# Optimization experiments

Measured on AMD Instinct MI355X. Metric: run time of the kernel, lower is better.

The kernel has to match this reference:

```python
import math
import jax, jax.numpy as jnp
import numpy as np

B, S, D_MODEL, H = 2, 2048, 1024, 16
D_HEAD = D_MODEL // H
NEG = -90000000000.0


def setup_inputs() -> dict:
    key = jax.random.key(0)
    ks = jax.random.split(key, 12)
    scale = 1.0 / math.sqrt(D_MODEL)
    return {
        "Q": jax.random.normal(ks[0], (B, S, D_MODEL), jnp.float32),
        "K": jax.random.normal(ks[1], (B, S, D_MODEL), jnp.float32),
        "V": jax.random.normal(ks[2], (B, S, D_MODEL), jnp.float32),
        "mask": jax.random.randint(ks[3], (B, 1, S, S), 0, 2).astype(bool),
        "Wq": jax.random.normal(ks[4], (D_MODEL, D_MODEL), jnp.float32) * scale,
        "bq": jnp.zeros((D_MODEL,), jnp.float32),
        "Wk": jax.random.normal(ks[5], (D_MODEL, D_MODEL), jnp.float32) * scale,
        "bk": jnp.zeros((D_MODEL,), jnp.float32),
        "Wv": jax.random.normal(ks[6], (D_MODEL, D_MODEL), jnp.float32) * scale,
        "bv": jnp.zeros((D_MODEL,), jnp.float32),
        "Wo": jax.random.normal(ks[7], (D_MODEL, D_MODEL), jnp.float32) * scale,
        "bo": jnp.zeros((D_MODEL,), jnp.float32),
    }


def _split_heads(x):
    # (B, S, D) -> (B, H, S, Dh)
    b, s, _ = x.shape
    return x.reshape(b, s, H, D_HEAD).transpose(0, 2, 1, 3)


def reference(Q, K, V, mask, Wq, bq, Wk, bk, Wv, bv, Wo, bo):
    q = _split_heads(Q @ Wq.T + bq)
    k = _split_heads(K @ Wk.T + bk)
    v = _split_heads(V @ Wv.T + bv)
    # scaled dot product with additive mask (mask.float() * -9e10)
    scores = jnp.einsum("bhqd,bhkd->bhqk", q, k) / math.sqrt(D_HEAD)
    scores = scores + mask.astype(scores.dtype) * NEG
    attn = jax.nn.softmax(scores, axis=-1)
    ctx = jnp.einsum("bhqk,bhkd->bhqd", attn, v)  # (B, H, S, Dh)
    ctx = ctx.transpose(0, 2, 1, 3).reshape(Q.shape[0], q.shape[2], D_MODEL)
    return ctx @ Wo.T + bo
```

## Files before the change

### kernel.cpp

```cpp
#include <hip/hip_runtime.h>
#include <hip/hip_bf16.h>


typedef __bf16 bf16x8 __attribute__((ext_vector_type(8)));
typedef __bf16 bf16x4 __attribute__((ext_vector_type(4)));
typedef float f32x4 __attribute__((ext_vector_type(4)));

#define S_LEN 2048
#define DM 1024
#define NH 16
#define DH 64
#define MROWS 4096

#define QSCALE 0.18033688011112042f

static __device__ __forceinline__ unsigned short f2bf(float f) {
    __bf16 b = (__bf16)f;
    unsigned short u; __builtin_memcpy(&u, &b, 2); return u;
}

static __device__ __forceinline__ float exp2_hw(float x) {
#if __has_builtin(__builtin_amdgcn_exp2f)
    return __builtin_amdgcn_exp2f(x);
#else
    float r; asm("v_exp_f32 %0, %1" : "=v"(r) : "v"(x)); return r;
#endif
}

static __device__ __forceinline__ unsigned cvtpk_bf16(float lo, float hi) {
    unsigned r;
    asm("v_cvt_pk_bf16_f32 %0, %1, %2" : "=v"(r) : "v"(lo), "v"(hi));
    return r;
}
static __device__ __forceinline__ void pl32swap(unsigned &x, unsigned &y) {
    asm volatile("v_permlane32_swap_b32 %0, %1" : "+v"(x), "+v"(y));
}
static __device__ __forceinline__ void pl16swap(unsigned &x, unsigned &y) {
    asm volatile("v_permlane16_swap_b32 %0, %1" : "+v"(x), "+v"(y));
}

static __device__ __forceinline__ bf16x8 cvt8(float4 a, float4 b) {
    bf16x8 o;
    o[0] = (__bf16)a.x; o[1] = (__bf16)a.y; o[2] = (__bf16)a.z; o[3] = (__bf16)a.w;
    o[4] = (__bf16)b.x; o[5] = (__bf16)b.y; o[6] = (__bf16)b.z; o[7] = (__bf16)b.w;
    return o;
}

__global__ __launch_bounds__(256)
void prep(const int* __restrict__ m, unsigned* __restrict__ mb,
          const float* __restrict__ Q, unsigned short* __restrict__ dQ,
          const float* __restrict__ K, unsigned short* __restrict__ dK,
          const float* __restrict__ V, unsigned short* __restrict__ dV,
          const float* __restrict__ W0, unsigned short* __restrict__ dW0,
          const float* __restrict__ W1, unsigned short* __restrict__ dW1,
          const float* __restrict__ W2, unsigned short* __restrict__ dW2,
          const float* __restrict__ W3, unsigned short* __restrict__ dW3)
{
    const int bx = blockIdx.x, tid = threadIdx.x;
    if (bx < 1024) {
        const int lane = tid & 63, w = tid >> 6;
        const int row = bx * 4 + w;
        const int* src = m + (size_t)row * S_LEN;
        unsigned* dst = mb + (size_t)row * (S_LEN / 32);
        for (int i = 0; i < 32; i++) {
            int v = src[i * 64 + lane];
            unsigned long long bm = __ballot(v != 0);
            if (lane == 0) { dst[i*2] = (unsigned)bm; dst[i*2+1] = (unsigned)(bm >> 32); }
        }
    } else if (bx < 7168) {
        int t = bx - 1024;
        int which = t >> 11;
        const float* s = which == 0 ? Q : which == 1 ? K : V;
        unsigned short* d = which == 0 ? dQ : which == 1 ? dK : dV;
        int i = ((t & 2047) * 256 + tid) * 8;
        float4 a = *(const float4*)(s + i);
        float4 b = *(const float4*)(s + i + 4);
        *(bf16x8*)(d + i) = cvt8(a, b);
    } else {
        int t = bx - 7168;
        int which = t >> 9;
        const float* s = which == 0 ? W0 : which == 1 ? W1 : which == 2 ? W2 : W3;
        unsigned short* d = which == 0 ? dW0 : which == 1 ? dW1 : which == 2 ? dW2 : dW3;
        int i = ((t & 511) * 256 + tid) * 8;
        float4 a = *(const float4*)(s + i);
        float4 b = *(const float4*)(s + i + 4);
        *(bf16x8*)(d + i) = cvt8(a, b);
    }
}

__global__ __launch_bounds__(256)
void gemm128(const unsigned short* __restrict__ X0, const unsigned short* __restrict__ X1,
             const unsigned short* __restrict__ X2,
             const unsigned short* __restrict__ W0, const unsigned short* __restrict__ W1,
             const unsigned short* __restrict__ W2,
             const float* __restrict__ b0, const float* __restrict__ b1,
             const float* __restrict__ b2,
             unsigned short* __restrict__ d0, unsigned short* __restrict__ d1,
             unsigned short* __restrict__ d2)
{
    __shared__ __align__(16) unsigned short As[2][128 * 32];
    __shared__ __align__(16) unsigned short Bs[2][128 * 32];

    const int bid = blockIdx.x + blockIdx.y * 8 + blockIdx.z * 256;
    const int xcd = bid & 7;
    const int t   = bid >> 3;
    const int z   = t >> 5;
    const int u   = t & 31;
    const int nt  = u & 7;
    const int mt  = xcd * 4 + (u >> 3);

    const unsigned short* X = z == 0 ? X0 : z == 1 ? X1 : X2;
    const unsigned short* W = z == 0 ? W0 : z == 1 ? W1 : W2;
    const float* bias        = z == 0 ? b0 : z == 1 ? b1 : b2;
    unsigned short* dstb     = z == 0 ? d0 : z == 1 ? d1 : d2;

    const int tid  = threadIdx.x;
    const int m0   = mt * 128;
    const int n0   = nt * 128;
    const int lane = tid & 63;
    const int w    = tid >> 6;
    const int wm   = (w >> 1) * 64, wn = (w & 1) * 64;
    const int lr   = lane & 15;
    const int lg   = lane >> 4;

    const int srow = tid >> 2, sc8 = (tid & 3) * 8;
    const int srow1 = (tid + 256) >> 2, sc81 = ((tid + 256) & 3) * 8;

    f32x4 acc[4][4];
#pragma unroll
    for (int i = 0; i < 4; i++)
#pragma unroll
        for (int j = 0; j < 4; j++) acc[i][j] = f32x4{0.f, 0.f, 0.f, 0.f};

#define G128_STAGE(buf, kk)                                                          \
    do {                                                                             \
        __builtin_amdgcn_global_load_lds(                                            \
            (const __attribute__((address_space(1))) unsigned*)&X[(size_t)(m0 + srow) * DM + (kk) + sc8],   \
            (__attribute__((address_space(3))) unsigned*)&As[buf][tid * 8], 16, 0, 0);                      \
        __builtin_amdgcn_global_load_lds(                                            \
            (const __attribute__((address_space(1))) unsigned*)&W[(size_t)(n0 + srow) * DM + (kk) + sc8],   \
            (__attribute__((address_space(3))) unsigned*)&Bs[buf][tid * 8], 16, 0, 0);                      \
        __builtin_amdgcn_global_load_lds(                                            \
            (const __attribute__((address_space(1))) unsigned*)&X[(size_t)(m0 + srow1) * DM + (kk) + sc81], \
            (__attribute__((address_space(3))) unsigned*)&As[buf][(tid + 256) * 8], 16, 0, 0);              \
        __builtin_amdgcn_global_load_lds(                                            \
            (const __attribute__((address_space(1))) unsigned*)&W[(size_t)(n0 + srow1) * DM + (kk) + sc81], \
            (__attribute__((address_space(3))) unsigned*)&Bs[buf][(tid + 256) * 8], 16, 0, 0);              \
    } while (0)

    G128_STAGE(0, 0);
    __syncthreads();

    for (int k0 = 0; k0 < DM; k0 += 32) {
        const int cur = (k0 >> 5) & 1;
        if (k0 + 32 < DM) G128_STAGE(cur ^ 1, k0 + 32);

        bf16x8 af[4], bfr[4];
#pragma unroll
        for (int mi = 0; mi < 4; mi++)
            af[mi] = *(const bf16x8*)(&As[cur][(wm + mi * 16 + lr) * 32 + lg * 8]);
#pragma unroll
        for (int ni = 0; ni < 4; ni++)
            bfr[ni] = *(const bf16x8*)(&Bs[cur][(wn + ni * 16 + lr) * 32 + lg * 8]);
#pragma unroll
        for (int mi = 0; mi < 4; mi++)
#pragma unroll
            for (int ni = 0; ni < 4; ni++)
                acc[mi][ni] = __builtin_amdgcn_mfma_f32_16x16x32_bf16(
                    af[mi], bfr[ni], acc[mi][ni], 0, 0, 0);
        __syncthreads();
    }
#undef G128_STAGE

#pragma unroll
    for (int mi = 0; mi < 4; mi++) {
#pragma unroll
        for (int ni = 0; ni < 4; ni++) {
            const int gcol = n0 + wn + ni * 16 + lr;
            const float bv = bias[gcol];
            const int grow0 = m0 + wm + mi * 16 + lg * 4;
            if (z == 2) {
                int b = grow0 >> 11, s = grow0 & (S_LEN - 1);
                int h = gcol >> 6, dh = gcol & 63;
                bf16x4 pk;
#pragma unroll
                for (int r = 0; r < 4; r++) pk[r] = (__bf16)(acc[mi][ni][r] + bv);
                size_t di = ((size_t)(b * NH + h) * DH + dh) * S_LEN + s;
                *(bf16x4*)(&dstb[di]) = pk;
            } else {
#pragma unroll
                for (int r = 0; r < 4; r++) {
                    int grow = grow0 + r;
                    float v = acc[mi][ni][r] + bv;
                    if (z == 0) v *= QSCALE;
                    int b = grow >> 11, s = grow & (S_LEN - 1);
                    int h = gcol >> 6, dh = gcol & 63;
                    dstb[((size_t)(b * NH + h) * S_LEN + s) * DH + dh] = f2bf(v);
                }
            }
        }
    }
}

__global__ __launch_bounds__(256, 2)
void gemm_out(const unsigned short* __restrict__ X, const unsigned short* __restrict__ W,
              const float* __restrict__ bias, float* __restrict__ dst)
{
    __shared__ __align__(16) unsigned short As[2][128 * 32];
    __shared__ __align__(16) unsigned short Bs[2][64 * 32];

    const int bid = blockIdx.x + blockIdx.y * 16;
    const int xcd = bid & 7;
    const int u   = bid >> 3;
    const int nt  = u & 15;
    const int mt  = xcd * 4 + (u >> 4);

    const int tid  = threadIdx.x;
    const int m0   = mt * 128;
    const int n0   = nt * 64;
    const int lane = tid & 63;
    const int w    = tid >> 6;
    const int wm   = (w >> 1) * 64, wn = (w & 1) * 32;
    const int lr   = lane & 15;
    const int lg   = lane >> 4;

    const int srow = tid >> 2, sc8 = (tid & 3) * 8;
    const int srow1 = (tid + 256) >> 2, sc81 = ((tid + 256) & 3) * 8;

    f32x4 acc[4][2];
#pragma unroll
    for (int i = 0; i < 4; i++)
#pragma unroll
        for (int j = 0; j < 2; j++) acc[i][j] = f32x4{0.f, 0.f, 0.f, 0.f};

#define GOUT_STAGE(buf, kk)                                                          \
    do {                                                                             \
        __builtin_amdgcn_global_load_lds(                                            \
            (const __attribute__((address_space(1))) unsigned*)&X[(size_t)(m0 + srow) * DM + (kk) + sc8],   \
            (__attribute__((address_space(3))) unsigned*)&As[buf][tid * 8], 16, 0, 0);                      \
        __builtin_amdgcn_global_load_lds(                                            \
            (const __attribute__((address_space(1))) unsigned*)&X[(size_t)(m0 + srow1) * DM + (kk) + sc81], \
            (__attribute__((address_space(3))) unsigned*)&As[buf][(tid + 256) * 8], 16, 0, 0);              \
        __builtin_amdgcn_global_load_lds(                                            \
            (const __attribute__((address_space(1))) unsigned*)&W[(size_t)(n0 + srow) * DM + (kk) + sc8],   \
            (__attribute__((address_space(3))) unsigned*)&Bs[buf][tid * 8], 16, 0, 0);                      \
    } while (0)

    GOUT_STAGE(0, 0);
    __syncthreads();

    for (int k0 = 0; k0 < DM; k0 += 32) {
        const int cur = (k0 >> 5) & 1;
        if (k0 + 32 < DM) GOUT_STAGE(cur ^ 1, k0 + 32);

        bf16x8 af[4], bfr[2];
#pragma unroll
        for (int mi = 0; mi < 4; mi++)
            af[mi] = *(const bf16x8*)(&As[cur][(wm + mi * 16 + lr) * 32 + lg * 8]);
#pragma unroll
        for (int ni = 0; ni < 2; ni++)
            bfr[ni] = *(const bf16x8*)(&Bs[cur][(wn + ni * 16 + lr) * 32 + lg * 8]);
#pragma unroll
        for (int mi = 0; mi < 4; mi++)
#pragma unroll
            for (int ni = 0; ni < 2; ni++)
                acc[mi][ni] = __builtin_amdgcn_mfma_f32_16x16x32_bf16(
                    af[mi], bfr[ni], acc[mi][ni], 0, 0, 0);
        __syncthreads();
    }
#undef GOUT_STAGE

#pragma unroll
    for (int mi = 0; mi < 4; mi++)
#pragma unroll
        for (int ni = 0; ni < 2; ni++) {
            const int gcol = n0 + wn + ni * 16 + lr;
            const float bv = bias[gcol];
            const int grow0 = m0 + wm + mi * 16 + lg * 4;
#pragma unroll
            for (int r = 0; r < 4; r++)
                dst[(size_t)(grow0 + r) * DM + gcol] = acc[mi][ni][r] + bv;
        }
}

__global__ __launch_bounds__(256, 2)
void attn(const unsigned short* __restrict__ q_ws,
          const unsigned short* __restrict__ k_ws,
          const unsigned short* __restrict__ vt_ws,
          const unsigned* __restrict__ mbits,
          unsigned short* __restrict__ ctx)
{
    __shared__ __align__(16) unsigned short Ks[2][64 * 72];
    __shared__ __align__(16) unsigned short Vs[2][64 * 72];
    const int tid = threadIdx.x, lane = tid & 63, w = tid >> 6;
    const int lr = lane & 15, lg = lane >> 4;

    const int i    = blockIdx.x;
    const int xcd  = i & 7;
    const int slot = i >> 3;
    const int bh   = xcd * 4 + (slot >> 4);
    const int qblk = slot & 15;
    const int b  = bh >> 4;
    const int h  = bh & 15;
    const int q0 = qblk * 128 + w * 32;
    const int qA = q0 + lr;
    const int qB = q0 + 16 + lr;

    const int srow = tid >> 3;
    const int sseg = tid & 7;

    const unsigned short* qh = q_ws + (size_t)bh * S_LEN * DH;
    const unsigned short* kh = k_ws + (size_t)bh * S_LEN * DH;
    const unsigned short* vh = vt_ws + (size_t)bh * DH * S_LEN;
    const unsigned* mrA = mbits + (size_t)(b * S_LEN + qA) * (S_LEN / 32);
    const unsigned* mrB = mbits + (size_t)(b * S_LEN + qB) * (S_LEN / 32);

    bf16x8 aqA[2], aqB[2];
#pragma unroll
    for (int c = 0; c < 2; c++) {
        aqA[c] = *(const bf16x8*)(&qh[(size_t)qA * DH + c * 32 + lg * 8]);
        aqB[c] = *(const bf16x8*)(&qh[(size_t)qB * DH + c * 32 + lg * 8]);
    }

    bf16x8 ones;
#pragma unroll
    for (int j = 0; j < 8; j++) ones[j] = (__bf16)1.0f;

    f32x4 accA[4], accB[4], accRA, accRB;
#pragma unroll
    for (int di = 0; di < 4; di++) {
        accA[di] = f32x4{0.f, 0.f, 0.f, 0.f};
        accB[di] = f32x4{0.f, 0.f, 0.f, 0.f};
    }
    accRA = f32x4{0.f, 0.f, 0.f, 0.f};
    accRB = f32x4{0.f, 0.f, 0.f, 0.f};

    uint4 kreg0, kreg1, vreg0, vreg1;
    kreg0 = *(const uint4*)(&kh[(size_t)(srow)      * DH + sseg * 8]);
    kreg1 = *(const uint4*)(&kh[(size_t)(srow + 32) * DH + sseg * 8]);
    vreg0 = *(const uint4*)(&vh[(size_t)(srow)      * S_LEN + sseg * 8]);
    vreg1 = *(const uint4*)(&vh[(size_t)(srow + 32) * S_LEN + sseg * 8]);
    *(uint4*)(&Ks[0][(srow)      * 72 + sseg * 8]) = kreg0;
    *(uint4*)(&Ks[0][(srow + 32) * 72 + sseg * 8]) = kreg1;
    *(uint4*)(&Vs[0][(srow)      * 72 + sseg * 8]) = vreg0;
    *(uint4*)(&Vs[0][(srow + 32) * 72 + sseg * 8]) = vreg1;
    kreg0 = *(const uint4*)(&kh[(size_t)(64 + srow)      * DH + sseg * 8]);
    kreg1 = *(const uint4*)(&kh[(size_t)(64 + srow + 32) * DH + sseg * 8]);
    vreg0 = *(const uint4*)(&vh[(size_t)(srow)      * S_LEN + 64 + sseg * 8]);
    vreg1 = *(const uint4*)(&vh[(size_t)(srow + 32) * S_LEN + 64 + sseg * 8]);
    __syncthreads();

    for (int it = 0; it < 32; it++) {
        const int cur = it & 1;
        const unsigned short* Kc = &Ks[cur][0];
        const unsigned short* Vc = &Vs[cur][0];
        if (it < 31) {
            unsigned short* Kn = &Ks[cur ^ 1][0];
            unsigned short* Vn = &Vs[cur ^ 1][0];
            *(uint4*)(&Kn[(srow)      * 72 + sseg * 8]) = kreg0;
            *(uint4*)(&Kn[(srow + 32) * 72 + sseg * 8]) = kreg1;
            *(uint4*)(&Vn[(srow)      * 72 + sseg * 8]) = vreg0;
            *(uint4*)(&Vn[(srow + 32) * 72 + sseg * 8]) = vreg1;
        }
        if (it < 30) {
            const int kn = (it + 2) * 64;
            kreg0 = *(const uint4*)(&kh[(size_t)(kn + srow)      * DH + sseg * 8]);
            kreg1 = *(const uint4*)(&kh[(size_t)(kn + srow + 32) * DH + sseg * 8]);
            vreg0 = *(const uint4*)(&vh[(size_t)(srow)      * S_LEN + kn + sseg * 8]);
            vreg1 = *(const uint4*)(&vh[(size_t)(srow + 32) * S_LEN + kn + sseg * 8]);
        }

        const uint2 mwA = *(const uint2*)(&mrA[it * 2]);
        const uint2 mwB = *(const uint2*)(&mrB[it * 2]);

        f32x4 sA[4], sB[4];
        __builtin_amdgcn_s_setprio(1);
#pragma unroll
        for (int ni = 0; ni < 4; ni++) {
            bf16x8 ak0 = *(const bf16x8*)(&Kc[(ni * 16 + lr) * 72 + lg * 8]);
            bf16x8 ak1 = *(const bf16x8*)(&Kc[(ni * 16 + lr) * 72 + 32 + lg * 8]);
            f32x4 tA = __builtin_amdgcn_mfma_f32_16x16x32_bf16(ak0, aqA[0], f32x4{0.f,0.f,0.f,0.f}, 0,0,0);
            tA = __builtin_amdgcn_mfma_f32_16x16x32_bf16(ak1, aqA[1], tA, 0,0,0);
            f32x4 tB = __builtin_amdgcn_mfma_f32_16x16x32_bf16(ak0, aqB[0], f32x4{0.f,0.f,0.f,0.f}, 0,0,0);
            tB = __builtin_amdgcn_mfma_f32_16x16x32_bf16(ak1, aqB[1], tB, 0,0,0);
            sA[ni] = tA; sB[ni] = tB;
        }
        __builtin_amdgcn_s_setprio(0);

#pragma unroll
        for (int ni = 0; ni < 4; ni++) {
            unsigned wA = (ni & 2) ? mwA.y : mwA.x;
            unsigned wB = (ni & 2) ? mwB.y : mwB.x;
            unsigned nibA = wA >> ((ni & 1) * 16 + lg * 4);
            unsigned nibB = wB >> ((ni & 1) * 16 + lg * 4);
#pragma unroll
            for (int r = 0; r < 4; r++) {
                float pA = exp2_hw(sA[ni][r]);
                float pB = exp2_hw(sB[ni][r]);
                sA[ni][r] = (nibA & (1u << r)) ? 0.f : pA;
                sB[ni][r] = (nibB & (1u << r)) ? 0.f : pB;
            }
        }

        unsigned wpA[8], wpB[8];
#pragma unroll
        for (int ni = 0; ni < 4; ni++) {
            wpA[ni*2]   = cvtpk_bf16(sA[ni][0], sA[ni][1]);
            wpA[ni*2+1] = cvtpk_bf16(sA[ni][2], sA[ni][3]);
            wpB[ni*2]   = cvtpk_bf16(sB[ni][0], sB[ni][1]);
            wpB[ni*2+1] = cvtpk_bf16(sB[ni][2], sB[ni][3]);
        }
#pragma unroll
        for (int c = 0; c < 2; c++) {
            pl32swap(wpA[c*4 + 0], wpA[c*4 + 2]);
            pl32swap(wpA[c*4 + 1], wpA[c*4 + 3]);
            pl16swap(wpA[c*4 + 0], wpA[c*4 + 2]);
            pl16swap(wpA[c*4 + 1], wpA[c*4 + 3]);
            pl32swap(wpB[c*4 + 0], wpB[c*4 + 2]);
            pl32swap(wpB[c*4 + 1], wpB[c*4 + 3]);
            pl16swap(wpB[c*4 + 0], wpB[c*4 + 2]);
            pl16swap(wpB[c*4 + 1], wpB[c*4 + 3]);
        }
        bf16x8 bpA0, bpA1, bpB0, bpB1;
        __builtin_memcpy(&bpA0, &wpA[0], 16);
        __builtin_memcpy(&bpA1, &wpA[4], 16);
        __builtin_memcpy(&bpB0, &wpB[0], 16);
        __builtin_memcpy(&bpB1, &wpB[4], 16);

        __builtin_amdgcn_s_setprio(1);
#pragma unroll
        for (int di = 0; di < 4; di++) {
            bf16x8 av0 = *(const bf16x8*)(&Vc[(di * 16 + lr) * 72 + lg * 8]);
            bf16x8 av1 = *(const bf16x8*)(&Vc[(di * 16 + lr) * 72 + 32 + lg * 8]);
            accA[di] = __builtin_amdgcn_mfma_f32_16x16x32_bf16(av0, bpA0, accA[di], 0, 0, 0);
            accA[di] = __builtin_amdgcn_mfma_f32_16x16x32_bf16(av1, bpA1, accA[di], 0, 0, 0);
            accB[di] = __builtin_amdgcn_mfma_f32_16x16x32_bf16(av0, bpB0, accB[di], 0, 0, 0);
            accB[di] = __builtin_amdgcn_mfma_f32_16x16x32_bf16(av1, bpB1, accB[di], 0, 0, 0);
        }
        accRA = __builtin_amdgcn_mfma_f32_16x16x32_bf16(ones, bpA0, accRA, 0, 0, 0);
        accRA = __builtin_amdgcn_mfma_f32_16x16x32_bf16(ones, bpA1, accRA, 0, 0, 0);
        accRB = __builtin_amdgcn_mfma_f32_16x16x32_bf16(ones, bpB0, accRB, 0, 0, 0);
        accRB = __builtin_amdgcn_mfma_f32_16x16x32_bf16(ones, bpB1, accRB, 0, 0, 0);
        __builtin_amdgcn_s_setprio(0);

        __syncthreads();
    }

    const float invA = 1.0f / fmaxf(accRA[0], 1e-37f);
    const float invB = 1.0f / fmaxf(accRB[0], 1e-37f);

    unsigned short* crowA = &ctx[((size_t)(b * S_LEN + qA)) * DM + h * DH];
    unsigned short* crowB = &ctx[((size_t)(b * S_LEN + qB)) * DM + h * DH];
#pragma unroll
    for (int di = 0; di < 4; di++) {
        bf16x4 oA, oB;
#pragma unroll
        for (int r = 0; r < 4; r++) {
            oA[r] = (__bf16)(accA[di][r] * invA);
            oB[r] = (__bf16)(accB[di][r] * invB);
        }
        *(bf16x4*)(&crowA[di * 16 + lg * 4]) = oA;
        *(bf16x4*)(&crowB[di * 16 + lg * 4]) = oB;
    }
}

extern "C" void kernel_launch(void* const* d_in, const int* in_sizes, int n_in,
                              void* d_out, int out_size, void* d_ws, size_t ws_size,
                              hipStream_t stream)
{
    (void)in_sizes; (void)n_in; (void)out_size; (void)ws_size;
    const float* Q  = (const float*)d_in[0];
    const float* K  = (const float*)d_in[1];
    const float* V  = (const float*)d_in[2];
    const int*   Mk = (const int*)d_in[3];
    const float* Wq = (const float*)d_in[4];
    const float* bq = (const float*)d_in[5];
    const float* Wk = (const float*)d_in[6];
    const float* bk = (const float*)d_in[7];
    const float* Wv = (const float*)d_in[8];
    const float* bv = (const float*)d_in[9];
    const float* Wo = (const float*)d_in[10];
    const float* bo = (const float*)d_in[11];

    const int NX = MROWS * DM;
    const int NW = DM * DM;

    unsigned short* q_ws  = (unsigned short*)d_ws;
    unsigned short* k_ws  = q_ws + (size_t)NX;
    unsigned short* vt_ws = k_ws + (size_t)NX;
    unsigned short* ctx   = vt_ws + (size_t)NX;
    unsigned*       mbits = (unsigned*)(ctx + (size_t)NX);
    unsigned short* Wbq   = (unsigned short*)(mbits + (size_t)MROWS * (S_LEN / 32));
    unsigned short* Wbk   = Wbq + (size_t)NW;
    unsigned short* Wbv   = Wbk + (size_t)NW;
    unsigned short* Wbo   = Wbv + (size_t)NW;
    unsigned short* Xbq   = Wbo + (size_t)NW;
    unsigned short* Xbk   = Xbq + (size_t)NX;
    unsigned short* Xbv   = Xbk + (size_t)NX;
    float* out = (float*)d_out;

    dim3 blk(256);
    prep<<<dim3(9216), blk, 0, stream>>>(Mk, mbits, Q, Xbq, K, Xbk, V, Xbv,
                                         Wq, Wbq, Wk, Wbk, Wv, Wbv, Wo, Wbo);

    gemm128<<<dim3(8, 32, 3), blk, 0, stream>>>(Xbq, Xbk, Xbv, Wbq, Wbk, Wbv,
                                                bq, bk, bv, q_ws, k_ws, vt_ws);

    attn<<<dim3(512), blk, 0, stream>>>(q_ws, k_ws, vt_ws, mbits, ctx);

    gemm_out<<<dim3(16, 32), blk, 0, stream>>>(ctx, Wbo, bo, out);
}
```

Before: 261.4 us.

## Use single-buffered BK=64 XOR-swizzled LDS tiles in projection GEMMs

Both the QKV projection GEMM and the output GEMM drop the double-buffered BK=32 staging in favour of one BK=64 LDS tile per operand. Columns are XOR-swizzled by row so that fragment reads avoid LDS bank conflicts, and the K loop takes half as many barrier-separated steps. Prefetch overlap within a block is lost, since loads now complete before compute, so gemm_out raises its occupancy hint to 4 blocks per CU to hide latency across blocks instead.

After: 264.0 us. No clear change (+1.0%).

```diff
diff --git a/kernel.cpp b/kernel.cpp
--- a/kernel.cpp
+++ b/kernel.cpp
@@ -98,8 +98,8 @@
              unsigned short* __restrict__ d0, unsigned short* __restrict__ d1,
              unsigned short* __restrict__ d2)
 {
-    __shared__ __align__(16) unsigned short As[2][128 * 32];
-    __shared__ __align__(16) unsigned short Bs[2][128 * 32];
+    __shared__ __align__(16) unsigned short As[128 * 64];
+    __shared__ __align__(16) unsigned short Bs[128 * 64];
 
     const int bid = blockIdx.x + blockIdx.y * 8 + blockIdx.z * 256;
     const int xcd = bid & 7;
@@ -122,9 +122,7 @@
     const int wm   = (w >> 1) * 64, wn = (w & 1) * 64;
     const int lr   = lane & 15;
     const int lg   = lane >> 4;
-
-    const int srow = tid >> 2, sc8 = (tid & 3) * 8;
-    const int srow1 = (tid + 256) >> 2, sc81 = ((tid + 256) & 3) * 8;
+    const int rx   = lr & 7;
 
     f32x4 acc[4][4];
 #pragma unroll
@@ -132,45 +130,42 @@
 #pragma unroll
         for (int j = 0; j < 4; j++) acc[i][j] = f32x4{0.f, 0.f, 0.f, 0.f};
 
-#define G128_STAGE(buf, kk)                                                          \
-    do {                                                                             \
-        __builtin_amdgcn_global_load_lds(                                            \
-            (const __attribute__((address_space(1))) unsigned*)&X[(size_t)(m0 + srow) * DM + (kk) + sc8],   \
-            (__attribute__((address_space(3))) unsigned*)&As[buf][tid * 8], 16, 0, 0);                      \
-        __builtin_amdgcn_global_load_lds(                                            \
-            (const __attribute__((address_space(1))) unsigned*)&W[(size_t)(n0 + srow) * DM + (kk) + sc8],   \
-            (__attribute__((address_space(3))) unsigned*)&Bs[buf][tid * 8], 16, 0, 0);                      \
-        __builtin_amdgcn_global_load_lds(                                            \
-            (const __attribute__((address_space(1))) unsigned*)&X[(size_t)(m0 + srow1) * DM + (kk) + sc81], \
-            (__attribute__((address_space(3))) unsigned*)&As[buf][(tid + 256) * 8], 16, 0, 0);              \
-        __builtin_amdgcn_global_load_lds(                                            \
-            (const __attribute__((address_space(1))) unsigned*)&W[(size_t)(n0 + srow1) * DM + (kk) + sc81], \
-            (__attribute__((address_space(3))) unsigned*)&Bs[buf][(tid + 256) * 8], 16, 0, 0);              \
-    } while (0)
-
-    G128_STAGE(0, 0);
-    __syncthreads();
-
-    for (int k0 = 0; k0 < DM; k0 += 32) {
-        const int cur = (k0 >> 5) & 1;
-        if (k0 + 32 < DM) G128_STAGE(cur ^ 1, k0 + 32);
-
-        bf16x8 af[4], bfr[4];
-#pragma unroll
-        for (int mi = 0; mi < 4; mi++)
-            af[mi] = *(const bf16x8*)(&As[cur][(wm + mi * 16 + lr) * 32 + lg * 8]);
-#pragma unroll
-        for (int ni = 0; ni < 4; ni++)
-            bfr[ni] = *(const bf16x8*)(&Bs[cur][(wn + ni * 16 + lr) * 32 + lg * 8]);
-#pragma unroll
-        for (int mi = 0; mi < 4; mi++)
-#pragma unroll
-            for (int ni = 0; ni < 4; ni++)
-                acc[mi][ni] = __builtin_amdgcn_mfma_f32_16x16x32_bf16(
-                    af[mi], bfr[ni], acc[mi][ni], 0, 0, 0);
+    for (int k0 = 0; k0 < DM; k0 += 64) {
         __syncthreads();
-    }
-#undef G128_STAGE
+#pragma unroll
+        for (int j = 0; j < 4; j++) {
+            int e = tid + j * 256;
+            int row = e >> 3;
+            int c8 = ((e & 7) ^ (row & 7)) * 8;
+            __builtin_amdgcn_global_load_lds(
+                (const __attribute__((address_space(1))) unsigned*)&X[(size_t)(m0 + row) * DM + k0 + c8],
+                (__attribute__((address_space(3))) unsigned*)&As[e * 8], 16, 0, 0);
+            __builtin_amdgcn_global_load_lds(
+                (const __attribute__((address_space(1))) unsigned*)&W[(size_t)(n0 + row) * DM + k0 + c8],
+                (__attribute__((address_space(3))) unsigned*)&Bs[e * 8], 16, 0, 0);
+        }
+        __syncthreads();
+#pragma unroll
+        for (int hh = 0; hh < 2; hh++) {
+            bf16x8 af[4], bfr[4];
+#pragma unroll
+            for (int mi = 0; mi < 4; mi++) {
+                int slot = (hh * 4 + lg) ^ rx;
+                af[mi] = *(const bf16x8*)(&As[(wm + mi * 16 + lr) * 64 + slot * 8]);
+            }
+#pragma unroll
+            for (int ni = 0; ni < 4; ni++) {
+                int slot = (hh * 4 + lg) ^ rx;
+                bfr[ni] = *(const bf16x8*)(&Bs[(wn + ni * 16 + lr) * 64 + slot * 8]);
+            }
+#pragma unroll
+            for (int mi = 0; mi < 4; mi++)
+#pragma unroll
+                for (int ni = 0; ni < 4; ni++)
+                    acc[mi][ni] = __builtin_amdgcn_mfma_f32_16x16x32_bf16(
+                        af[mi], bfr[ni], acc[mi][ni], 0, 0, 0);
+        }
+    }
 
 #pragma unroll
     for (int mi = 0; mi < 4; mi++) {
@@ -202,12 +197,12 @@
     }
 }
 
-__global__ __launch_bounds__(256, 2)
+__global__ __launch_bounds__(256, 4)
 void gemm_out(const unsigned short* __restrict__ X, const unsigned short* __restrict__ W,
               const float* __restrict__ bias, float* __restrict__ dst)
 {
-    __shared__ __align__(16) unsigned short As[2][128 * 32];
-    __shared__ __align__(16) unsigned short Bs[2][64 * 32];
+    __shared__ __align__(16) unsigned short As[128 * 64];
+    __shared__ __align__(16) unsigned short Bs[64 * 64];
 
     const int bid = blockIdx.x + blockIdx.y * 16;
     const int xcd = bid & 7;
@@ -223,9 +218,7 @@
     const int wm   = (w >> 1) * 64, wn = (w & 1) * 32;
     const int lr   = lane & 15;
     const int lg   = lane >> 4;
-
-    const int srow = tid >> 2, sc8 = (tid & 3) * 8;
-    const int srow1 = (tid + 256) >> 2, sc81 = ((tid + 256) & 3) * 8;
+    const int rx   = lr & 7;
 
     f32x4 acc[4][2];
 #pragma unroll
@@ -233,43 +226,45 @@
 #pragma unroll
         for (int j = 0; j < 2; j++) acc[i][j] = f32x4{0.f, 0.f, 0.f, 0.f};
 
-#define GOUT_STAGE(buf, kk)                                                          \
-    do {                                                                             \
-        __builtin_amdgcn_global_load_lds(                                            \
-            (const __attribute__((address_space(1))) unsigned*)&X[(size_t)(m0 + srow) * DM + (kk) + sc8],   \
-            (__attribute__((address_space(3))) unsigned*)&As[buf][tid * 8], 16, 0, 0);                      \
-        __builtin_amdgcn_global_load_lds(                                            \
-            (const __attribute__((address_space(1))) unsigned*)&X[(size_t)(m0 + srow1) * DM + (kk) + sc81], \
-            (__attribute__((address_space(3))) unsigned*)&As[buf][(tid + 256) * 8], 16, 0, 0);              \
-        __builtin_amdgcn_global_load_lds(                                            \
-            (const __attribute__((address_space(1))) unsigned*)&W[(size_t)(n0 + srow) * DM + (kk) + sc8],   \
-            (__attribute__((address_space(3))) unsigned*)&Bs[buf][tid * 8], 16, 0, 0);                      \
-    } while (0)
-
-    GOUT_STAGE(0, 0);
-    __syncthreads();
-
-    for (int k0 = 0; k0 < DM; k0 += 32) {
-        const int cur = (k0 >> 5) & 1;
-        if (k0 + 32 < DM) GOUT_STAGE(cur ^ 1, k0 + 32);
-
-        bf16x8 af[4], bfr[2];
-#pragma unroll
-        for (int mi = 0; mi < 4; mi++)
-            af[mi] = *(const bf16x8*)(&As[cur][(wm + mi * 16 + lr) * 32 + lg * 8]);
-#pragma unroll
-        for (int ni = 0; ni < 2; ni++)
-            bfr[ni] = *(const bf16x8*)(&Bs[cur][(wn + ni * 16 + lr) * 32 + lg * 8]);
-#pragma unroll
-        for (int mi = 0; mi < 4; mi++)
+    for (int k0 = 0; k0 < DM; k0 += 64) {
+        __syncthreads();
+#pragma unroll
+        for (int j = 0; j < 4; j++) {
+            int e = tid + j * 256;
+            int row = e >> 3;
+            int c8 = ((e & 7) ^ (row & 7)) * 8;
+            __builtin_amdgcn_global_load_lds(
+                (const __attribute__((address_space(1))) unsigned*)&X[(size_t)(m0 + row) * DM + k0 + c8],
+                (__attribute__((address_space(3))) unsigned*)&As[e * 8], 16, 0, 0);
+        }
+#pragma unroll
+        for (int j = 0; j < 2; j++) {
+            int e = tid + j * 256;
+            int row = e >> 3;
+            int c8 = ((e & 7) ^ (row & 7)) * 8;
+            __builtin_amdgcn_global_load_lds(
+                (const __attribute__((address_space(1))) unsigned*)&W[(size_t)(n0 + row) * DM + k0 + c8],
+                (__attribute__((address_space(3))) unsigned*)&Bs[e * 8], 16, 0, 0);
+        }
+        __syncthreads();
+#pragma unroll
+        for (int hh = 0; hh < 2; hh++) {
+            bf16x8 af[4], bfr[2];
+            int slot = (hh * 4 + lg) ^ rx;
+#pragma unroll
+            for (int mi = 0; mi < 4; mi++)
+                af[mi] = *(const bf16x8*)(&As[(wm + mi * 16 + lr) * 64 + slot * 8]);
 #pragma unroll
             for (int ni = 0; ni < 2; ni++)
-                acc[mi][ni] = __builtin_amdgcn_mfma_f32_16x16x32_bf16(
-                    af[mi], bfr[ni], acc[mi][ni], 0, 0, 0);
-        __syncthreads();
-    }
-#undef GOUT_STAGE
-
+                bfr[ni] = *(const bf16x8*)(&Bs[(wn + ni * 16 + lr) * 64 + slot * 8]);
+#pragma unroll
+            for (int mi = 0; mi < 4; mi++)
+#pragma unroll
+                for (int ni = 0; ni < 2; ni++)
+                    acc[mi][ni] = __builtin_amdgcn_mfma_f32_16x16x32_bf16(
+                        af[mi], bfr[ni], acc[mi][ni], 0, 0, 0);
+        }
+    }
 #pragma unroll
     for (int mi = 0; mi < 4; mi++)
 #pragma unroll
```
